# Kernel optimization log

Hardware: AMD Instinct MI355X
Metric: run time of the kernel (lower is better)

Reference implementation:

```python
import jax, jax.numpy as jnp
import numpy as np

ENTITY_DIM = 128; REL_DIM = 128; D1 = 8; D2 = 16
NC = 32; K = 3
H_OUT = D1 - K + 1; W_OUT = D2 - K + 1
FEAT = NC * H_OUT * W_OUT            # 2688
NUM_ENT = 40943; NUM_REL = 474; B = 256; HID = 256
EPS = 1e-5


def _bn(x, axes):
    # torch BatchNorm train mode with default gamma=1, beta=0 (biased variance)
    m = x.mean(axes, keepdims=True)
    v = x.var(axes, keepdims=True)
    return (x - m) * jax.lax.rsqrt(v + EPS)


def setup_inputs() -> dict:
    key = jax.random.key(0)
    ks = jax.random.split(key, 12)
    s = lambda k, shp, fan: jax.random.normal(k, shp, jnp.float32) / np.float32(np.sqrt(fan))
    return {
        "e1": jax.random.randint(ks[0], (B,), 0, NUM_ENT),
        "r": jax.random.randint(ks[1], (B,), 0, NUM_REL),
        "entity_emb": s(ks[2], (NUM_ENT, ENTITY_DIM), ENTITY_DIM),
        "relation_emb": s(ks[3], (NUM_REL, REL_DIM), REL_DIM),
        "convw_w1": s(ks[4], (REL_DIM, HID), REL_DIM),
        "convw_w2": s(ks[5], (HID, NC * K * K), HID),
        "convb_w1": s(ks[6], (REL_DIM, HID), REL_DIM),
        "convb_w2": s(ks[7], (HID, NC), HID),
        "fcw_w1": s(ks[8], (REL_DIM, HID), REL_DIM),
        "fcw_w2": s(ks[9], (HID, FEAT * ENTITY_DIM), HID),
        "fcb_w1": s(ks[10], (REL_DIM, HID), REL_DIM),
        "fcb_w2": s(ks[11], (HID, ENTITY_DIM), HID),
        "b": jnp.zeros((NUM_ENT,), jnp.float32),
    }


def reference(e1, r, entity_emb, relation_emb,
              convw_w1, convw_w2, convb_w1, convb_w2,
              fcw_w1, fcw_w2, fcb_w1, fcb_w2, b):
    E1 = entity_emb[e1].reshape(B, 1, D1, D2)      # [B,1,8,16]
    R = relation_emb[r]                            # [B,128]
    E2 = entity_emb                                # [NUM_ENT,128]

    x = _bn(E1, (0, 2, 3))                         # bn0 over batch+spatial, 1 channel

    # ContextualParameterGenerator: Linear -> ReLU -> Linear (no bias, eval dropout)
    cpg = lambda w1, w2: jax.nn.relu(R @ w1) @ w2

    filt = cpg(convw_w1, convw_w2).reshape(B * NC, 1, K, K)   # per-sample conv filters
    cbias = cpg(convb_w1, convb_w2)                            # [B,NC]

    # per-sample conv2d as a grouped conv: groups=B, each group has 1 in-ch, NC out-ch
    out = jax.lax.conv_general_dilated(
        x.reshape(1, B, D1, D2), filt,
        window_strides=(1, 1), padding='VALID',
        feature_group_count=B,
        dimension_numbers=('NCHW', 'OIHW', 'NCHW'))           # [1,B*NC,6,14]
    X = out.reshape(B, NC, H_OUT, W_OUT) + cbias[:, :, None, None]
    X = jax.nn.relu(X).reshape(B, FEAT)

    fc_w = cpg(fcw_w1, fcw_w2).reshape(B, FEAT, ENTITY_DIM)   # per-sample FC weights
    X = jnp.einsum('ij,ijk->ik', X, fc_w) + cpg(fcb_w1, fcb_w2)

    X = jax.nn.relu(_bn(X, (0,)))                              # bn2 + relu
    return jax.nn.sigmoid(X @ E2.T + b)                        # [B,NUM_ENT]
```

## Files before the change

kernel.cpp:

```cpp
#include <hip/hip_runtime.h>
#include <cstdint>
#include <cstddef>

#define BATCH 256
#define ED 128
#define NC 32
#define HO 6
#define WO 14
#define FEAT 2688
#define HID 256
#define NE 40943
#define EPS 1e-5f
#define W2COLS 344064

typedef __attribute__((ext_vector_type(4))) float f32x4;
typedef __attribute__((ext_vector_type(8))) short short8;
typedef __attribute__((ext_vector_type(4))) short short4v;

__device__ __forceinline__ ushort f2bf(float f) {
    uint32_t u = __builtin_bit_cast(uint32_t, f);
    u = (u + 0x7FFFu + ((u >> 16) & 1u)) >> 16;
    return (ushort)u;
}

__global__ void k0_bn0(const int* __restrict__ e1, const float* __restrict__ emb,
                       float* __restrict__ stats) {
    __shared__ float s1[1024], s2[1024];
    int t = threadIdx.x;
    int i = t >> 2, p = (t & 3) * 32;
    const float* row = emb + (size_t)e1[i] * ED + p;
    float a = 0.f, b = 0.f;
#pragma unroll
    for (int q = 0; q < 32; ++q) { float v = row[q]; a += v; b += v * v; }
    s1[t] = a; s2[t] = b;
    __syncthreads();
    for (int s = 512; s > 0; s >>= 1) {
        if (t < s) { s1[t] += s1[t + s]; s2[t] += s2[t + s]; }
        __syncthreads();
    }
    if (t == 0) {
        float m = s1[0] / 32768.f;
        float v = s2[0] / 32768.f - m * m;
        stats[0] = m;
        stats[1] = rsqrtf(v + EPS);
    }
}

__global__ void k1_hidden(const int* __restrict__ r, const float* __restrict__ rel,
                          const float* __restrict__ w1a, const float* __restrict__ w1b,
                          const float* __restrict__ w1c, const float* __restrict__ w1d,
                          float* __restrict__ H) {
    int head = blockIdx.x >> 8;
    int i = blockIdx.x & 255;
    int u = threadIdx.x;
    __shared__ float R[128];
    if (u < 128) R[u] = rel[(size_t)r[i] * 128 + u];
    __syncthreads();
    const float* w1 = head == 0 ? w1a : head == 1 ? w1b : head == 2 ? w1c : w1d;
    float acc = 0.f;
#pragma unroll 8
    for (int d = 0; d < 128; ++d) acc += R[d] * w1[d * 256 + u];
    H[((size_t)head * 256 + i) * 256 + u] = fmaxf(acc, 0.f);
}

__global__ void k2_heads(const float* __restrict__ H,
                         const float* __restrict__ w2f, const float* __restrict__ w2b,
                         const float* __restrict__ w2fcb,
                         float* __restrict__ filt, float* __restrict__ cbias,
                         float* __restrict__ fcb) {
    int i = blockIdx.x;
    int t = threadIdx.x;
    __shared__ float h0[256], h1[256], h3[256];
    if (t < 256) {
        h0[t] = H[(size_t)(0 * 256 + i) * 256 + t];
        h1[t] = H[(size_t)(1 * 256 + i) * 256 + t];
        h3[t] = H[(size_t)(3 * 256 + i) * 256 + t];
    }
    __syncthreads();
    if (t < 288) {
        float a = 0.f;
#pragma unroll 8
        for (int u = 0; u < 256; ++u) a += h0[u] * w2f[u * 288 + t];
        filt[i * 288 + t] = a;
    } else if (t < 320) {
        int c = t - 288;
        float a = 0.f;
#pragma unroll 8
        for (int u = 0; u < 256; ++u) a += h1[u] * w2b[u * 32 + c];
        cbias[i * 32 + c] = a;
    } else if (t < 448) {
        int c = t - 320;
        float a = 0.f;
#pragma unroll 8
        for (int u = 0; u < 256; ++u) a += h3[u] * w2fcb[u * 128 + c];
        fcb[i * 128 + c] = a;
    }
}

__global__ void k3_conv(const int* __restrict__ e1, const float* __restrict__ emb,
                        const float* __restrict__ stats, const float* __restrict__ filt,
                        const float* __restrict__ cbias, ushort* __restrict__ Xc) {
    int i = blockIdx.x, t = threadIdx.x;
    __shared__ float x[128], f[288], cb[32];
    float mean = stats[0], rstd = stats[1];
    if (t < 128) x[t] = (emb[(size_t)e1[i] * 128 + t] - mean) * rstd;
    if (t < 32) cb[t] = cbias[i * 32 + t];
    for (int o = t; o < 288; o += 256) f[o] = filt[i * 288 + o];
    __syncthreads();
    for (int o = t; o < FEAT; o += 256) {
        int c = o / 84, rem = o % 84;
        int y = rem / 14, xw = rem % 14;
        float acc = cb[c];
        const float* fc = &f[c * 9];
#pragma unroll
        for (int dy = 0; dy < 3; ++dy)
#pragma unroll
            for (int dx = 0; dx < 3; ++dx)
                acc += x[(y + dy) * 16 + (xw + dx)] * fc[dy * 3 + dx];
        Xc[(size_t)i * FEAT + o] = f2bf(fmaxf(acc, 0.f));
    }
}

__global__ __launch_bounds__(512, 4) void k4_gemm(const ushort* __restrict__ Xc,
                                                  const float* __restrict__ W2,
                                                  float* __restrict__ T) {
    int h = blockIdx.x >> 1;
    int kh = (blockIdx.x & 1) * 64;
    int tid = threadIdx.x, lane = tid & 63, wave = tid >> 6;
    int l15 = lane & 15, l4 = lane >> 4;
    __shared__ __align__(16) ushort Bt[2][64 * 36];
    const float* Brow = W2 + (size_t)h * W2COLS + kh;

    int kk = tid & 63;
    int jg = tid >> 6;
    const float* src = Brow + (size_t)(jg * 4) * 128 + kk;

    f32x4 acc[2][4];
#pragma unroll
    for (int mt = 0; mt < 2; ++mt)
#pragma unroll
        for (int nt = 0; nt < 4; ++nt)
#pragma unroll
            for (int q = 0; q < 4; ++q) acc[mt][nt][q] = 0.f;

    float p0[4], p1[4];
#pragma unroll
    for (int q = 0; q < 4; ++q) p0[q] = src[(size_t)q * 128];
#pragma unroll
    for (int q = 0; q < 4; ++q) p1[q] = src[(size_t)(32 + q) * 128];

    for (int s = 0; s < 84; ++s) {
        short4v w4;
#pragma unroll
        for (int q = 0; q < 4; ++q) w4[q] = (short)f2bf(p0[q]);
        *(short4v*)&Bt[s & 1][kk * 36 + jg * 4] = w4;
        __syncthreads();
#pragma unroll
        for (int q = 0; q < 4; ++q) p0[q] = p1[q];
        if (s + 2 < 84) {
            int jb = (s + 2) * 32;
#pragma unroll
            for (int q = 0; q < 4; ++q) p1[q] = src[(size_t)(jb + q) * 128];
        }
        int j0 = s * 32;
        short8 bf[4];
#pragma unroll
        for (int nt = 0; nt < 4; ++nt)
            bf[nt] = *(const short8*)&Bt[s & 1][(nt * 16 + l15) * 36 + l4 * 8];
        short8 af[2];
#pragma unroll
        for (int mt = 0; mt < 2; ++mt) {
            int i = wave * 32 + mt * 16 + l15;
            af[mt] = *(const short8*)(Xc + (size_t)i * FEAT + j0 + l4 * 8);
        }
#pragma unroll
        for (int mt = 0; mt < 2; ++mt)
#pragma unroll
            for (int nt = 0; nt < 4; ++nt)
                acc[mt][nt] = __builtin_amdgcn_mfma_f32_16x16x32_bf16(
                    af[mt], bf[nt], acc[mt][nt], 0, 0, 0);
    }
#pragma unroll
    for (int mt = 0; mt < 2; ++mt)
#pragma unroll
        for (int nt = 0; nt < 4; ++nt) {
            int row0 = wave * 32 + mt * 16 + l4 * 4;
            int col = kh + nt * 16 + l15;
#pragma unroll
            for (int rr = 0; rr < 4; ++rr)
                T[((size_t)h * 256 + row0 + rr) * 128 + col] = acc[mt][nt][rr];
        }
}

__global__ void k5_stage2(const float* __restrict__ T, const float* __restrict__ Hfc,
                          const float* __restrict__ fcb, float* __restrict__ X) {
    int i = blockIdx.x, k = threadIdx.x;
    const float* hp = Hfc + (size_t)i * 256;
    const float* tp = T + (size_t)i * 128 + k;
    float acc = fcb[i * 128 + k];
#pragma unroll 16
    for (int h = 0; h < 256; ++h) acc += hp[h] * tp[(size_t)h * 32768];
    X[i * 128 + k] = acc;
}

__global__ void k6_bn2(const float* __restrict__ X, ushort* __restrict__ Xn) {
    int k = blockIdx.x;
    int i = threadIdx.x;
    __shared__ float s1[256], s2[256];
    float v = X[i * 128 + k];
    s1[i] = v; s2[i] = v * v;
    __syncthreads();
    for (int s = 128; s > 0; s >>= 1) {
        if (i < s) { s1[i] += s1[i + s]; s2[i] += s2[i + s]; }
        __syncthreads();
    }
    float m = s1[0] / 256.f;
    float var = s2[0] / 256.f - m * m;
    float rstd = rsqrtf(var + EPS);
    Xn[i * 128 + k] = f2bf(fmaxf((v - m) * rstd, 0.f));
}

__global__ __launch_bounds__(256) void k7_final(const ushort* __restrict__ Xn,
                                                const float* __restrict__ E2,
                                                const float* __restrict__ bias,
                                                float* __restrict__ out) {
    int eb = blockIdx.x * 64;
    int lane = threadIdx.x & 63, wave = threadIdx.x >> 6;
    int l15 = lane & 15, l4 = lane >> 4;
    int i0 = wave * 64;

    f32x4 acc[4][4];
#pragma unroll
    for (int mt = 0; mt < 4; ++mt)
#pragma unroll
        for (int nt = 0; nt < 4; ++nt)
#pragma unroll
            for (int q = 0; q < 4; ++q) acc[mt][nt][q] = 0.f;

#pragma unroll
    for (int ks = 0; ks < 4; ++ks) {
        int k0 = ks * 32 + l4 * 8;
        short8 a[4];
#pragma unroll
        for (int mt = 0; mt < 4; ++mt) {
            int i = i0 + mt * 16 + l15;
            a[mt] = *(const short8*)(Xn + (size_t)i * 128 + k0);
        }
        short8 b[4];
#pragma unroll
        for (int nt = 0; nt < 4; ++nt) {
            int e = eb + nt * 16 + l15;
            int ec = e < NE ? e : NE - 1;
            const float* rp = E2 + (size_t)ec * 128 + k0;
            short8 tv;
#pragma unroll
            for (int q = 0; q < 8; ++q) tv[q] = (short)f2bf(rp[q]);
            b[nt] = tv;
        }
#pragma unroll
        for (int mt = 0; mt < 4; ++mt)
#pragma unroll
            for (int nt = 0; nt < 4; ++nt)
                acc[mt][nt] = __builtin_amdgcn_mfma_f32_16x16x32_bf16(
                    a[mt], b[nt], acc[mt][nt], 0, 0, 0);
    }
#pragma unroll
    for (int nt = 0; nt < 4; ++nt) {
        int e = eb + nt * 16 + l15;
        bool ok = e < NE;
        float bb = bias[e < NE ? e : NE - 1];
#pragma unroll
        for (int mt = 0; mt < 4; ++mt) {
            int row0 = i0 + mt * 16 + l4 * 4;
#pragma unroll
            for (int rr = 0; rr < 4; ++rr) {
                float v = acc[mt][nt][rr] + bb;
                float sg = 1.f / (1.f + __expf(-v));
                if (ok) out[(size_t)(row0 + rr) * NE + e] = sg;
            }
        }
    }
}

extern "C" void kernel_launch(void* const* d_in, const int* in_sizes, int n_in,
                              void* d_out, int out_size, void* d_ws, size_t ws_size,
                              hipStream_t stream) {
    const int* e1 = (const int*)d_in[0];
    const int* r = (const int*)d_in[1];
    const float* emb = (const float*)d_in[2];
    const float* rel = (const float*)d_in[3];
    const float* convw_w1 = (const float*)d_in[4];
    const float* convw_w2 = (const float*)d_in[5];
    const float* convb_w1 = (const float*)d_in[6];
    const float* convb_w2 = (const float*)d_in[7];
    const float* fcw_w1 = (const float*)d_in[8];
    const float* fcw_w2 = (const float*)d_in[9];
    const float* fcb_w1 = (const float*)d_in[10];
    const float* fcb_w2 = (const float*)d_in[11];
    const float* bvec = (const float*)d_in[12];
    float* out = (float*)d_out;

    char* ws = (char*)d_ws;
    float* stats = (float*)(ws + 0);
    float* H = (float*)(ws + 256);
    float* filt = (float*)(ws + 1048832);
    float* cbias = (float*)(ws + 1343744);
    float* fcbv = (float*)(ws + 1376512);
    ushort* Xc = (ushort*)(ws + 1507584);
    float* T = (float*)(ws + 2883840);
    float* X = (float*)(ws + 36438272);
    ushort* Xn = (ushort*)(ws + 36569344);

    k0_bn0<<<1, 1024, 0, stream>>>(e1, emb, stats);
    k1_hidden<<<1024, 256, 0, stream>>>(r, rel, convw_w1, convb_w1, fcw_w1, fcb_w1, H);
    k2_heads<<<256, 512, 0, stream>>>(H, convw_w2, convb_w2, fcb_w2, filt, cbias, fcbv);
    k3_conv<<<256, 256, 0, stream>>>(e1, emb, stats, filt, cbias, Xc);
    k4_gemm<<<512, 512, 0, stream>>>(Xc, fcw_w2, T);
    k5_stage2<<<256, 128, 0, stream>>>(T, H + 2 * 65536, fcbv, X);
    k6_bn2<<<128, 256, 0, stream>>>(X, Xn);
    k7_final<<<640, 256, 0, stream>>>(Xn, emb, bvec, out);
}
```

Baseline: 665.3 us.

## Fuse hypernet and conv kernels, store intermediate T in bf16, vectorize E2 loads

Merges the hidden-layer, head and per-sample conv kernels into one per-sample block, so the filters, conv bias and hidden activations stay in shared memory and do not round-trip through global memory. The stage-1 GEMM output T is now written in bf16, which halves the traffic of the large intermediate that k5 reads. The final GEMM loads entity rows as float4 vectors. Rounding T to bf16 adds extra precision loss, and the fused kernel runs only 256 blocks.

```diff
diff --git a/kernel.cpp b/kernel.cpp
--- a/kernel.cpp
+++ b/kernel.cpp
@@ -5,8 +5,6 @@
 #define BATCH 256
 #define ED 128
 #define NC 32
-#define HO 6
-#define WO 14
 #define FEAT 2688
 #define HID 256
 #define NE 40943
@@ -21,6 +19,10 @@
     uint32_t u = __builtin_bit_cast(uint32_t, f);
     u = (u + 0x7FFFu + ((u >> 16) & 1u)) >> 16;
     return (ushort)u;
+}
+__device__ __forceinline__ float bf2f(ushort u) {
+    uint32_t v = ((uint32_t)u) << 16;
+    return __builtin_bit_cast(float, v);
 }
 
 __global__ void k0_bn0(const int* __restrict__ e1, const float* __restrict__ emb,
@@ -46,84 +48,76 @@
     }
 }
 
-__global__ void k1_hidden(const int* __restrict__ r, const float* __restrict__ rel,
-                          const float* __restrict__ w1a, const float* __restrict__ w1b,
-                          const float* __restrict__ w1c, const float* __restrict__ w1d,
-                          float* __restrict__ H) {
-    int head = blockIdx.x >> 8;
-    int i = blockIdx.x & 255;
-    int u = threadIdx.x;
+__global__ __launch_bounds__(512) void k12_fused(
+        const int* __restrict__ e1, const int* __restrict__ r,
+        const float* __restrict__ rel, const float* __restrict__ stats,
+        const float* __restrict__ emb,
+        const float* __restrict__ w1a, const float* __restrict__ w1b,
+        const float* __restrict__ w1c, const float* __restrict__ w1d,
+        const float* __restrict__ w2f, const float* __restrict__ w2b,
+        const float* __restrict__ w2fcb,
+        float* __restrict__ Hfc, float* __restrict__ fcbv,
+        ushort* __restrict__ Xc) {
+    int i = blockIdx.x, t = threadIdx.x;
     __shared__ float R[128];
-    if (u < 128) R[u] = rel[(size_t)r[i] * 128 + u];
-    __syncthreads();
-    const float* w1 = head == 0 ? w1a : head == 1 ? w1b : head == 2 ? w1c : w1d;
-    float acc = 0.f;
+    __shared__ float hh[4][256];
+    __shared__ float sf[288], scb[32], sx[128];
+    if (t < 128) R[t] = rel[(size_t)r[i] * 128 + t];
+    __syncthreads();
+#pragma unroll
+    for (int rep = 0; rep < 2; ++rep) {
+        int idx = rep * 512 + t;
+        int head = idx >> 8, u = idx & 255;
+        const float* w1 = head == 0 ? w1a : head == 1 ? w1b : head == 2 ? w1c : w1d;
+        float acc = 0.f;
 #pragma unroll 8
-    for (int d = 0; d < 128; ++d) acc += R[d] * w1[d * 256 + u];
-    H[((size_t)head * 256 + i) * 256 + u] = fmaxf(acc, 0.f);
-}
-
-__global__ void k2_heads(const float* __restrict__ H,
-                         const float* __restrict__ w2f, const float* __restrict__ w2b,
-                         const float* __restrict__ w2fcb,
-                         float* __restrict__ filt, float* __restrict__ cbias,
-                         float* __restrict__ fcb) {
-    int i = blockIdx.x;
-    int t = threadIdx.x;
-    __shared__ float h0[256], h1[256], h3[256];
-    if (t < 256) {
-        h0[t] = H[(size_t)(0 * 256 + i) * 256 + t];
-        h1[t] = H[(size_t)(1 * 256 + i) * 256 + t];
-        h3[t] = H[(size_t)(3 * 256 + i) * 256 + t];
-    }
-    __syncthreads();
+        for (int d = 0; d < 128; ++d) acc += R[d] * w1[d * 256 + u];
+        hh[head][u] = fmaxf(acc, 0.f);
+    }
+    __syncthreads();
+    if (t < 256) Hfc[(size_t)i * 256 + t] = hh[2][t];
     if (t < 288) {
         float a = 0.f;
 #pragma unroll 8
-        for (int u = 0; u < 256; ++u) a += h0[u] * w2f[u * 288 + t];
-        filt[i * 288 + t] = a;
+        for (int u = 0; u < 256; ++u) a += hh[0][u] * w2f[u * 288 + t];
+        sf[t] = a;
     } else if (t < 320) {
         int c = t - 288;
         float a = 0.f;
 #pragma unroll 8
-        for (int u = 0; u < 256; ++u) a += h1[u] * w2b[u * 32 + c];
-        cbias[i * 32 + c] = a;
+        for (int u = 0; u < 256; ++u) a += hh[1][u] * w2b[u * 32 + c];
+        scb[c] = a;
     } else if (t < 448) {
         int c = t - 320;
         float a = 0.f;
 #pragma unroll 8
-        for (int u = 0; u < 256; ++u) a += h3[u] * w2fcb[u * 128 + c];
-        fcb[i * 128 + c] = a;
-    }
-}
-
-__global__ void k3_conv(const int* __restrict__ e1, const float* __restrict__ emb,
-                        const float* __restrict__ stats, const float* __restrict__ filt,
-                        const float* __restrict__ cbias, ushort* __restrict__ Xc) {
-    int i = blockIdx.x, t = threadIdx.x;
-    __shared__ float x[128], f[288], cb[32];
-    float mean = stats[0], rstd = stats[1];
-    if (t < 128) x[t] = (emb[(size_t)e1[i] * 128 + t] - mean) * rstd;
-    if (t < 32) cb[t] = cbias[i * 32 + t];
-    for (int o = t; o < 288; o += 256) f[o] = filt[i * 288 + o];
-    __syncthreads();
-    for (int o = t; o < FEAT; o += 256) {
+        for (int u = 0; u < 256; ++u) a += hh[3][u] * w2fcb[u * 128 + c];
+        fcbv[i * 128 + c] = a;
+    } else {
+        int q = t - 448;
+        float m = stats[0], rs = stats[1];
+        const float* xr = emb + (size_t)e1[i] * 128;
+        sx[q] = (xr[q] - m) * rs;
+        sx[q + 64] = (xr[q + 64] - m) * rs;
+    }
+    __syncthreads();
+    for (int o = t; o < FEAT; o += 512) {
         int c = o / 84, rem = o % 84;
         int y = rem / 14, xw = rem % 14;
-        float acc = cb[c];
-        const float* fc = &f[c * 9];
+        float acc = scb[c];
+        const float* fc = &sf[c * 9];
 #pragma unroll
         for (int dy = 0; dy < 3; ++dy)
 #pragma unroll
             for (int dx = 0; dx < 3; ++dx)
-                acc += x[(y + dy) * 16 + (xw + dx)] * fc[dy * 3 + dx];
+                acc += sx[(y + dy) * 16 + (xw + dx)] * fc[dy * 3 + dx];
         Xc[(size_t)i * FEAT + o] = f2bf(fmaxf(acc, 0.f));
     }
 }
 
 __global__ __launch_bounds__(512, 4) void k4_gemm(const ushort* __restrict__ Xc,
                                                   const float* __restrict__ W2,
-                                                  float* __restrict__ T) {
+                                                  ushort* __restrict__ T) {
     int h = blockIdx.x >> 1;
     int kh = (blockIdx.x & 1) * 64;
     int tid = threadIdx.x, lane = tid & 63, wave = tid >> 6;
@@ -188,18 +182,18 @@
             int col = kh + nt * 16 + l15;
 #pragma unroll
             for (int rr = 0; rr < 4; ++rr)
-                T[((size_t)h * 256 + row0 + rr) * 128 + col] = acc[mt][nt][rr];
-        }
-}
-
-__global__ void k5_stage2(const float* __restrict__ T, const float* __restrict__ Hfc,
-                          const float* __restrict__ fcb, float* __restrict__ X) {
+                T[((size_t)h * 256 + row0 + rr) * 128 + col] = f2bf(acc[mt][nt][rr]);
+        }
+}
+
+__global__ void k5_stage2(const ushort* __restrict__ T, const float* __restrict__ Hfc,
+                          const float* __restrict__ fcbv, float* __restrict__ X) {
     int i = blockIdx.x, k = threadIdx.x;
     const float* hp = Hfc + (size_t)i * 256;
-    const float* tp = T + (size_t)i * 128 + k;
-    float acc = fcb[i * 128 + k];
+    const ushort* tp = T + (size_t)i * 128 + k;
+    float acc = fcbv[i * 128 + k];
 #pragma unroll 16
-    for (int h = 0; h < 256; ++h) acc += hp[h] * tp[(size_t)h * 32768];
+    for (int h = 0; h < 256; ++h) acc += hp[h] * bf2f(tp[(size_t)h * 32768]);
     X[i * 128 + k] = acc;
 }
 
@@ -251,10 +245,13 @@
         for (int nt = 0; nt < 4; ++nt) {
             int e = eb + nt * 16 + l15;
             int ec = e < NE ? e : NE - 1;
-            const float* rp = E2 + (size_t)ec * 128 + k0;
+            const f32x4* rp = (const f32x4*)(E2 + (size_t)ec * 128 + k0);
+            f32x4 v0 = rp[0], v1 = rp[1];
             short8 tv;
 #pragma unroll
-            for (int q = 0; q < 8; ++q) tv[q] = (short)f2bf(rp[q]);
+            for (int q = 0; q < 4; ++q) tv[q] = (short)f2bf(v0[q]);
+#pragma unroll
+            for (int q = 0; q < 4; ++q) tv[q + 4] = (short)f2bf(v1[q]);
             b[nt] = tv;
         }
 #pragma unroll
@@ -302,21 +299,20 @@
 
     char* ws = (char*)d_ws;
     float* stats = (float*)(ws + 0);
-    float* H = (float*)(ws + 256);
-    float* filt = (float*)(ws + 1048832);
-    float* cbias = (float*)(ws + 1343744);
-    float* fcbv = (float*)(ws + 1376512);
-    ushort* Xc = (ushort*)(ws + 1507584);
-    float* T = (float*)(ws + 2883840);
-    float* X = (float*)(ws + 36438272);
-    ushort* Xn = (ushort*)(ws + 36569344);
+    float* Hfc = (float*)(ws + 256);
+    float* fcbv = (float*)(ws + 262400);
+    ushort* Xc = (ushort*)(ws + 393472);
+    ushort* T = (ushort*)(ws + 1769728);
+    float* X = (float*)(ws + 18546944);
+    ushort* Xn = (ushort*)(ws + 18678016);
 
     k0_bn0<<<1, 1024, 0, stream>>>(e1, emb, stats);
-    k1_hidden<<<1024, 256, 0, stream>>>(r, rel, convw_w1, convb_w1, fcw_w1, fcb_w1, H);
-    k2_heads<<<256, 512, 0, stream>>>(H, convw_w2, convb_w2, fcb_w2, filt, cbias, fcbv);
-    k3_conv<<<256, 256, 0, stream>>>(e1, emb, stats, filt, cbias, Xc);
+    k12_fused<<<256, 512, 0, stream>>>(e1, r, rel, stats, emb,
+                                       convw_w1, convb_w1, fcw_w1, fcb_w1,
+                                       convw_w2, convb_w2, fcb_w2,
+                                       Hfc, fcbv, Xc);
     k4_gemm<<<512, 512, 0, stream>>>(Xc, fcw_w2, T);
-    k5_stage2<<<256, 128, 0, stream>>>(T, H + 2 * 65536, fcbv, X);
+    k5_stage2<<<256, 128, 0, stream>>>(T, Hfc, fcbv, X);
     k6_bn2<<<128, 256, 0, stream>>>(X, Xn);
     k7_final<<<640, 256, 0, stream>>>(Xn, emb, bvec, out);
 }
```

Result: no change. 664.1 us (-0.2%).
